# Kernel tuning notes

Measured on AMD Instinct MI355X. Metric: run time of the kernel, lower is better.

The kernel has to match this reference:

```python
import jax, jax.numpy as jnp
import numpy as np

HIDDEN = 2048
KEY_DIM = 2048
NUM_HEADS = 16
EPS = 1e-05


def rms_norm(x, w, eps=EPS):
    ms = jnp.mean(x * x, axis=-1, keepdims=True)
    return x * jax.lax.rsqrt(ms + eps) * w


def setup_inputs() -> dict:
    key = jax.random.key(0)
    ks = jax.random.split(key, 6)
    bound = 1.0 / np.sqrt(HIDDEN)  # kaiming-uniform-ish scale
    x = jax.random.normal(ks[0], (2, 2048, HIDDEN), dtype=jnp.float32)
    rms_w = jnp.ones((HIDDEN,), dtype=jnp.float32)
    Wq = jax.random.uniform(ks[1], (HIDDEN, KEY_DIM), jnp.float32, -bound, bound)
    Wk = jax.random.uniform(ks[2], (HIDDEN, KEY_DIM), jnp.float32, -bound, bound)
    Wv = jax.random.uniform(ks[3], (HIDDEN, KEY_DIM), jnp.float32, -bound, bound)
    Wo = jax.random.uniform(ks[4], (KEY_DIM, HIDDEN), jnp.float32, -bound, bound)
    return {"x": x, "rms_w": rms_w, "Wq": Wq, "Wk": Wk, "Wv": Wv, "Wo": Wo}


def reference(x, rms_w, Wq, Wk, Wv, Wo):
    B, S, _ = x.shape
    residual = x
    xn = rms_norm(x, rms_w)
    # project and split heads: [B,S,H,Dh]
    q = (xn @ Wq).reshape(B, S, NUM_HEADS, KEY_DIM // NUM_HEADS)
    k = (xn @ Wk).reshape(B, S, NUM_HEADS, KEY_DIM // NUM_HEADS)
    v = (xn @ Wv).reshape(B, S, NUM_HEADS, KEY_DIM // NUM_HEADS)
    # NOTE: original scales by 1/sqrt(key_dim), not head_dim — kept faithful
    scale = 1.0 / jnp.sqrt(jnp.float32(KEY_DIM))
    scores = jnp.einsum('bshd,bthd->bhst', q, k) * scale  # [B,H,S,S]
    causal = jnp.tril(jnp.ones((S, S), dtype=bool))
    scores = jnp.where(causal[None, None], scores, -jnp.inf)
    probs = jax.nn.softmax(scores, axis=-1)  # stable max-subtract internally
    out = jnp.einsum('bhst,bthd->bshd', probs, v).reshape(B, S, KEY_DIM)
    return out @ Wo + residual
```

## Files before the change

kernel.cpp:

```cpp
#include <hip/hip_runtime.h>
#include <math.h>

typedef __attribute__((ext_vector_type(8))) short bf16x8;
typedef __attribute__((ext_vector_type(4))) float f32x4;
typedef __attribute__((ext_vector_type(16))) float f32x16;

#define HID 2048
#define SEQ 2048
#define NH  16
#define DH  128
#define QS_LOG2E 0.0318793607f

__device__ __forceinline__ ushort f2bf(float f) {
  union { float f; unsigned u; } v; v.f = f;
  unsigned r = v.u + 0x7fffu + ((v.u >> 16) & 1u);
  return (ushort)(r >> 16);
}

__device__ __forceinline__ void gload16(const ushort* g, ushort* l) {
  __builtin_amdgcn_global_load_lds((const __attribute__((address_space(1))) void*)g,
                                   (__attribute__((address_space(3))) void*)l,
                                   16, 0, 0);
}

#define VMCNT(n) asm volatile("s_waitcnt vmcnt(" #n ")" ::: "memory")
#define ABAR()   asm volatile("s_barrier" ::: "memory")

__global__ __launch_bounds__(256) void k_transpose4(const float* __restrict__ W0,
                                                    const float* __restrict__ W1,
                                                    const float* __restrict__ W2,
                                                    const float* __restrict__ W3,
                                                    ushort* __restrict__ T0,
                                                    ushort* __restrict__ T3) {
  __shared__ float t[32][33];
  int z = blockIdx.z;
  const float* W = (z == 0) ? W0 : (z == 1) ? W1 : (z == 2) ? W2 : W3;
  ushort* Wt = (z == 3) ? T3 : (T0 + (size_t)z * 2048 * 2048);
  int n0 = blockIdx.x * 32, k0 = blockIdx.y * 32;
  int tx = threadIdx.x, ty = threadIdx.y;
  for (int i = ty; i < 32; i += 8)
    t[i][tx] = W[(size_t)(k0 + i) * HID + n0 + tx];
  __syncthreads();
  for (int i = ty; i < 32; i += 8)
    Wt[(size_t)(n0 + i) * HID + k0 + tx] = f2bf(t[tx][i]);
}

__global__ __launch_bounds__(256) void k_rmsnorm(const float* __restrict__ x,
                                                 const float* __restrict__ w,
                                                 ushort* __restrict__ xn) {
  int row = blockIdx.x;
  const float* xr = x + (size_t)row * HID;
  int base = threadIdx.x * 8;
  float4 a = *(const float4*)(xr + base);
  float4 c = *(const float4*)(xr + base + 4);
  float ss = a.x*a.x + a.y*a.y + a.z*a.z + a.w*a.w
           + c.x*c.x + c.y*c.y + c.z*c.z + c.w*c.w;
  #pragma unroll
  for (int off = 32; off > 0; off >>= 1) ss += __shfl_xor(ss, off);
  __shared__ float red[4];
  if ((threadIdx.x & 63) == 0) red[threadIdx.x >> 6] = ss;
  __syncthreads();
  float tot = red[0] + red[1] + red[2] + red[3];
  float sc = rsqrtf(tot * (1.0f / HID) + 1e-5f);
  float4 wa = *(const float4*)(w + base);
  float4 wc = *(const float4*)(w + base + 4);
  ushort h[8];
  h[0] = f2bf(a.x * sc * wa.x); h[1] = f2bf(a.y * sc * wa.y);
  h[2] = f2bf(a.z * sc * wa.z); h[3] = f2bf(a.w * sc * wa.w);
  h[4] = f2bf(c.x * sc * wc.x); h[5] = f2bf(c.y * sc * wc.y);
  h[6] = f2bf(c.z * sc * wc.z); h[7] = f2bf(c.w * sc * wc.w);
  int4 pk;
  pk.x = h[0] | ((int)h[1] << 16);
  pk.y = h[2] | ((int)h[3] << 16);
  pk.z = h[4] | ((int)h[5] << 16);
  pk.w = h[6] | ((int)h[7] << 16);
  *(int4*)&xn[(size_t)row * HID + base] = pk;
}

__global__ __launch_bounds__(512, 2) void k_gemm10(const ushort* __restrict__ A,
                                                   const ushort* __restrict__ Bt,
                                                   ushort* __restrict__ obf,
                                                   ushort* __restrict__ vt) {
  constexpr int K = 2048;
  __shared__ ushort lds[8][8192];
  const int tid = threadIdx.x;
  const int lane = tid & 63, w = tid >> 6;
  const int wm = w >> 2, wn = w & 3;
  const int g = lane >> 4, l15 = lane & 15;
  const int bm = blockIdx.y, bn = blockIdx.x;

  f32x4 acc[8][4];
  #pragma unroll
  for (int i = 0; i < 8; ++i)
    #pragma unroll
    for (int j = 0; j < 4; ++j) acc[i][j] = f32x4{0.f, 0.f, 0.f, 0.f};

  const ushort* pA[2][2];
  const ushort* pB[2][2];
  #pragma unroll
  for (int kh = 0; kh < 2; ++kh)
    #pragma unroll
    for (int L = 0; L < 2; ++L) {
      int row = L * 128 + w * 16 + (lane >> 2);
      int ck = (lane & 3) ^ ((row >> 1) & 3);
      pA[kh][L] = &A[(size_t)(bm * 256 + row) * K + kh * 32 + ck * 8];
      pB[kh][L] = &Bt[(size_t)(bn * 256 + row) * K + kh * 32 + ck * 8];
    }

  auto STAGE = [&](int buf, int kh) {
    ushort* ra = lds[buf * 4 + kh * 2 + 0];
    ushort* rb = lds[buf * 4 + kh * 2 + 1];
    #pragma unroll
    for (int L = 0; L < 2; ++L) {
      gload16(pA[kh][L], ra + (L * 8 + w) * 512);
      pA[kh][L] += 64;
    }
    #pragma unroll
    for (int L = 0; L < 2; ++L) {
      gload16(pB[kh][L], rb + (L * 8 + w) * 512);
      pB[kh][L] += 64;
    }
  };

  auto COMP = [&](int buf, int kh) {
    const ushort* ra = lds[buf * 4 + kh * 2 + 0];
    const ushort* rb = lds[buf * 4 + kh * 2 + 1];
    bf16x8 aF[8], bF[4];
    #pragma unroll
    for (int i = 0; i < 8; ++i) {
      int row = wm * 128 + i * 16 + l15;
      aF[i] = *(const bf16x8*)&ra[row * 32 + ((g ^ ((row >> 1) & 3)) * 8)];
    }
    #pragma unroll
    for (int j = 0; j < 4; ++j) {
      int row = wn * 64 + j * 16 + l15;
      bF[j] = *(const bf16x8*)&rb[row * 32 + ((g ^ ((row >> 1) & 3)) * 8)];
    }
    __builtin_amdgcn_s_setprio(1);
    #pragma unroll
    for (int i = 0; i < 8; ++i)
      #pragma unroll
      for (int j = 0; j < 4; ++j)
        acc[i][j] = __builtin_amdgcn_mfma_f32_16x16x32_bf16(aF[i], bF[j], acc[i][j], 0, 0, 0);
    __builtin_amdgcn_s_setprio(0);
  };

  STAGE(0, 0); STAGE(0, 1); STAGE(1, 0);

  #pragma unroll 1
  for (int t = 0; t < 30; ++t) {
    const int b = t & 1, nb = b ^ 1;
    VMCNT(8); ABAR();
    STAGE(nb, 1);
    COMP(b, 0);
    VMCNT(8); ABAR();
    STAGE(b, 0);
    COMP(b, 1);
  }
  VMCNT(8); ABAR(); STAGE(1, 1); COMP(0, 0);
  VMCNT(8); ABAR();               COMP(0, 1);
  VMCNT(4); ABAR(); COMP(1, 0);
  VMCNT(0); ABAR(); COMP(1, 1);

  int rbase = bm * 256 + wm * 128 + g * 4;
  int cbase = bn * 256 + wn * 64 + l15;
  if (bn < 16) {
    const float sc = (bn < 8) ? QS_LOG2E : 1.0f;
    #pragma unroll
    for (int i = 0; i < 8; ++i) {
      #pragma unroll
      for (int j = 0; j < 4; ++j) {
        int col = cbase + j * 16;
        #pragma unroll
        for (int r = 0; r < 4; ++r) {
          int row = rbase + i * 16 + r;
          obf[(size_t)row * 4096 + col] = f2bf(acc[i][j][r] * sc);
        }
      }
    }
  } else {
    #pragma unroll
    for (int i = 0; i < 8; ++i) {
      int rowb = rbase + i * 16;
      int b = rowb >> 11, s = rowb & 2047;
      #pragma unroll
      for (int j = 0; j < 4; ++j) {
        int nv = cbase + j * 16 - 4096;
        int h = nv >> 7, d = nv & 127;
        uint lo = (uint)f2bf(acc[i][j][0]) | ((uint)f2bf(acc[i][j][1]) << 16);
        uint hi = (uint)f2bf(acc[i][j][2]) | ((uint)f2bf(acc[i][j][3]) << 16);
        uint2 pk = {lo, hi};
        *(uint2*)&vt[(size_t)((b * NH + h) * DH + d) * SEQ + s] = pk;
      }
    }
  }
}

__global__ __launch_bounds__(256) void k_gemm7o(const ushort* __restrict__ A,
                                                const ushort* __restrict__ Bt,
                                                float* __restrict__ ofl,
                                                const float* __restrict__ resid,
                                                int K) {
  __shared__ ushort sA[128 * 64];
  __shared__ ushort sB[128 * 64];
  const int tid = threadIdx.x;
  const int lane = tid & 63, w = tid >> 6;
  const int wr = w >> 1, wc = w & 1;
  const int bm = blockIdx.y, bn = blockIdx.x;
  const int g = lane >> 4, l15 = lane & 15;
  f32x4 acc[4][4];
  #pragma unroll
  for (int i = 0; i < 4; ++i)
    #pragma unroll
    for (int j = 0; j < 4; ++j) acc[i][j] = f32x4{0.f, 0.f, 0.f, 0.f};

  const ushort* ap[4];
  const ushort* bp[4];
  ushort* la[4];
  ushort* lb[4];
  #pragma unroll
  for (int c = 0; c < 4; ++c) {
    int id = (w * 4 + c) * 64 + lane;
    int r = id >> 3, ck = id & 7;
    int ke = (ck ^ (r & 7)) * 8;
    ap[c] = &A[(size_t)(bm * 128 + r) * K + ke];
    bp[c] = &Bt[(size_t)(bn * 128 + r) * K + ke];
    la[c] = ((ushort*)sA) + (w * 4 + c) * 512;
    lb[c] = ((ushort*)sB) + (w * 4 + c) * 512;
  }

  const int nt = K / 64;
  #pragma unroll 1
  for (int t = 0; t < nt; ++t) {
    #pragma unroll
    for (int c = 0; c < 4; ++c) {
      gload16(ap[c], la[c]);
      gload16(bp[c], lb[c]);
      ap[c] += 64;
      bp[c] += 64;
    }
    __syncthreads();
    #pragma unroll
    for (int kk = 0; kk < 2; ++kk) {
      bf16x8 aF[4], bF[4];
      #pragma unroll
      for (int i = 0; i < 4; ++i) {
        int row = wr * 64 + i * 16 + l15;
        int cp = (kk * 4 + g) ^ (lane & 7);
        aF[i] = *(const bf16x8*)&sA[row * 64 + cp * 8];
      }
      #pragma unroll
      for (int j = 0; j < 4; ++j) {
        int row = wc * 64 + j * 16 + l15;
        int cp = (kk * 4 + g) ^ (lane & 7);
        bF[j] = *(const bf16x8*)&sB[row * 64 + cp * 8];
      }
      #pragma unroll
      for (int i = 0; i < 4; ++i)
        #pragma unroll
        for (int j = 0; j < 4; ++j)
          acc[i][j] = __builtin_amdgcn_mfma_f32_16x16x32_bf16(aF[i], bF[j], acc[i][j], 0, 0, 0);
    }
    __syncthreads();
  }

  int rbase = bm * 128 + wr * 64 + g * 4;
  int cbase = bn * 128 + wc * 64 + l15;
  #pragma unroll
  for (int i = 0; i < 4; ++i) {
    #pragma unroll
    for (int j = 0; j < 4; ++j) {
      int col = cbase + j * 16;
      #pragma unroll
      for (int r = 0; r < 4; ++r) {
        int row = rbase + i * 16 + r;
        ofl[(size_t)row * HID + col] = acc[i][j][r] + resid[(size_t)row * HID + col];
      }
    }
  }
}

__global__ __launch_bounds__(256, 2) void k_attn5(const ushort* __restrict__ qk,
                                                  const ushort* __restrict__ vt,
                                                  ushort* __restrict__ aout) {
  __shared__ ushort sK[64 * 128];
  __shared__ ushort sV[128 * 64];
  const int tid = threadIdx.x;
  const int lane = tid & 63, w = tid >> 6;
  const int h2 = lane >> 5;
  const int l31 = lane & 31;
  const int bid = blockIdx.x;
  const int t = bid >> 3;
  const int u = t & 31, v = t >> 5;
  const int bh = (bid & 7) + 8 * (u & 3);
  const int qblk = v ? 15 - (u >> 2) : (u >> 2);
  const int b = bh >> 4, hh = bh & 15;
  const int q0w = qblk * 128 + w * 32;

  bf16x8 qf[8];
  {
    const ushort* qbase = qk + (size_t)(b * SEQ + q0w + l31) * 4096 + hh * DH;
    #pragma unroll
    for (int kk = 0; kk < 8; ++kk) qf[kk] = *(const bf16x8*)&qbase[kk * 16 + h2 * 8];
  }

  const ushort* kp[4];
  const ushort* vp[4];
  ushort* lk[4];
  ushort* lv[4];
  #pragma unroll
  for (int c = 0; c < 4; ++c) {
    int id = (w * 4 + c) * 64 + lane;
    int kr = id >> 4, ck = id & 15;
    kp[c] = qk + (size_t)(b * SEQ + kr) * 4096 + 2048 + hh * DH + ((ck ^ (kr & 7)) * 8);
    int dr = id >> 3, cv = id & 7;
    vp[c] = vt + (size_t)(bh * DH + dr) * SEQ + ((cv ^ (dr & 7)) * 8);
    lk[c] = ((ushort*)sK) + (size_t)(w * 4 + c) * 512;
    lv[c] = ((ushort*)sV) + (size_t)(w * 4 + c) * 512;
  }

  f32x16 accO[4];
  #pragma unroll
  for (int i = 0; i < 4; ++i)
    #pragma unroll
    for (int r = 0; r < 16; ++r) accO[i][r] = 0.f;
  float l_r = 0.f;

  const int ntile = 2 * qblk + 2;
  #pragma unroll 1
  for (int tt = 0; tt < ntile; ++tt) {
    const int t0 = tt * 64;
    #pragma unroll
    for (int c = 0; c < 4; ++c) {
      gload16(kp[c], lk[c]);
      gload16(vp[c], lv[c]);
      kp[c] += 64 * 4096;
      vp[c] += 64;
    }
    __syncthreads();

    if (t0 <= q0w + 31) {
      f32x16 accS[2];
      #pragma unroll
      for (int i = 0; i < 2; ++i)
        #pragma unroll
        for (int r = 0; r < 16; ++r) accS[i][r] = 0.f;
      #pragma unroll
      for (int kt = 0; kt < 2; ++kt) {
        const int row = kt * 32 + l31;
        #pragma unroll
        for (int kk = 0; kk < 8; ++kk) {
          const int cp = (kk * 2 + h2) ^ (lane & 7);
          bf16x8 kf = *(const bf16x8*)&sK[row * 128 + cp * 8];
          accS[kt] = __builtin_amdgcn_mfma_f32_32x32x16_bf16(kf, qf[kk], accS[kt], 0, 0, 0);
        }
      }
      float rs = 0.f;
      if (t0 + 63 <= q0w) {
        #pragma unroll
        for (int kt = 0; kt < 2; ++kt)
          #pragma unroll
          for (int r = 0; r < 16; ++r) {
            float p = __builtin_amdgcn_exp2f(accS[kt][r]);
            rs += p;
            accS[kt][r] = p;
          }
      } else {
        const int qa = q0w + l31;
        #pragma unroll
        for (int kt = 0; kt < 2; ++kt)
          #pragma unroll
          for (int r = 0; r < 16; ++r) {
            int ka = t0 + kt * 32 + (r & 3) + 8 * (r >> 2) + 4 * h2;
            float p = (ka <= qa) ? __builtin_amdgcn_exp2f(accS[kt][r]) : 0.f;
            rs += p;
            accS[kt][r] = p;
          }
      }
      rs += __shfl_xor(rs, 32);
      l_r += rs;

      uint W[2][4][2];
      #pragma unroll
      for (int kt = 0; kt < 2; ++kt)
        #pragma unroll
        for (int bq = 0; bq < 4; ++bq)
          #pragma unroll
          for (int w2 = 0; w2 < 2; ++w2) {
            uint u0 = __float_as_uint(accS[kt][bq * 4 + w2 * 2]);
            uint u1 = __float_as_uint(accS[kt][bq * 4 + w2 * 2 + 1]);
            W[kt][bq][w2] = (u0 >> 16) | (u1 & 0xffff0000u);
          }
      #pragma unroll
      for (int kc = 0; kc < 4; ++kc) {
        const int kt = kc >> 1, pq = kc & 1;
        uint X0 = W[kt][2 * pq][0],     X1 = W[kt][2 * pq][1];
        uint Y0 = W[kt][2 * pq + 1][0], Y1 = W[kt][2 * pq + 1][1];
        uint sx0 = (uint)__shfl_xor((int)X0, 32);
        uint sx1 = (uint)__shfl_xor((int)X1, 32);
        uint sy0 = (uint)__shfl_xor((int)Y0, 32);
        uint sy1 = (uint)__shfl_xor((int)Y1, 32);
        union { uint u[4]; bf16x8 v; } pu;
        pu.u[0] = h2 ? sy0 : X0;
        pu.u[1] = h2 ? sy1 : X1;
        pu.u[2] = h2 ? Y0 : sx0;
        pu.u[3] = h2 ? Y1 : sx1;
        #pragma unroll
        for (int ds = 0; ds < 4; ++ds) {
          const int dr = ds * 32 + l31;
          const int cp = (kc * 2 + h2) ^ (lane & 7);
          bf16x8 vf = *(const bf16x8*)&sV[dr * 64 + cp * 8];
          accO[ds] = __builtin_amdgcn_mfma_f32_32x32x16_bf16(pu.v, vf, accO[ds], 0, 0, 0);
        }
      }
    }
    __syncthreads();
  }

  float linv = 1.f / l_r;
  #pragma unroll
  for (int r = 0; r < 16; ++r) {
    int qrel = (r & 3) + 8 * (r >> 2) + 4 * h2;
    float li = __shfl(linv, qrel);
    #pragma unroll
    for (int ds = 0; ds < 4; ++ds) {
      aout[(size_t)(b * SEQ + q0w + qrel) * HID + hh * DH + ds * 32 + l31] =
          f2bf(accO[ds][r] * li);
    }
  }
}

extern "C" void kernel_launch(void* const* d_in, const int* in_sizes, int n_in,
                              void* d_out, int out_size, void* d_ws, size_t ws_size,
                              hipStream_t stream) {
  const float* x     = (const float*)d_in[0];
  const float* rms_w = (const float*)d_in[1];
  const float* Wq    = (const float*)d_in[2];
  const float* Wk    = (const float*)d_in[3];
  const float* Wv    = (const float*)d_in[4];
  const float* Wo    = (const float*)d_in[5];
  float* out = (float*)d_out;

  char* ws = (char*)d_ws;
  ushort* WqkvT = (ushort*)ws; ws += (size_t)6144 * 2048 * 2;
  ushort* WoT   = (ushort*)ws; ws += (size_t)2048 * 2048 * 2;
  ushort* xn    = (ushort*)ws; ws += (size_t)4096 * 2048 * 2;
  ushort* qkbuf = (ushort*)ws; ws += (size_t)4096 * 4096 * 2;
  ushort* vt    = (ushort*)ws; ws += (size_t)4096 * 2048 * 2;
  ushort* aout  = (ushort*)ws; ws += (size_t)4096 * 2048 * 2;

  k_transpose4<<<dim3(64, 64, 4), dim3(32, 8), 0, stream>>>(Wq, Wk, Wv, Wo, WqkvT, WoT);

  k_rmsnorm<<<4096, 256, 0, stream>>>(x, rms_w, xn);

  k_gemm10<<<dim3(24, 16), 512, 0, stream>>>(xn, WqkvT, qkbuf, vt);

  k_attn5<<<512, 256, 0, stream>>>(qkbuf, vt, aout);

  k_gemm7o<<<dim3(16, 32), 256, 0, stream>>>(aout, WoT, out, x, 2048);
}
```

Baseline: 260.3 us.

## Split QKV GEMM compute into half-tiles interleaved with global-to-LDS staging

Restructures the QKV projection GEMM main loop so each K-step is split into two halves. Each half reads part of the A fragments from LDS, issues half of the next global-to-LDS loads, then runs 16 MFMAs, with extra barriers and explicit lgkmcnt waits between phases. The aim is to spread memory issue across the compute so loads and MFMAs overlap better, and to hold fewer A fragments in registers at once. The cost is many more s_barrier instructions per iteration, which can add stalls across the 8 waves.

```diff
diff --git a/kernel.cpp b/kernel.cpp
--- a/kernel.cpp
+++ b/kernel.cpp
@@ -24,6 +24,8 @@
 }
 
 #define VMCNT(n) asm volatile("s_waitcnt vmcnt(" #n ")" ::: "memory")
+#define LGKM0()  do { asm volatile("s_waitcnt lgkmcnt(0)" ::: "memory"); \
+                      __builtin_amdgcn_sched_barrier(0); } while (0)
 #define ABAR()   asm volatile("s_barrier" ::: "memory")
 
 __global__ __launch_bounds__(256) void k_transpose4(const float* __restrict__ W0,
@@ -77,7 +79,7 @@
   *(int4*)&xn[(size_t)row * HID + base] = pk;
 }
 
-__global__ __launch_bounds__(512, 2) void k_gemm10(const ushort* __restrict__ A,
+__global__ __launch_bounds__(512, 2) void k_gemm11(const ushort* __restrict__ A,
                                                    const ushort* __restrict__ Bt,
                                                    ushort* __restrict__ obf,
                                                    ushort* __restrict__ vt) {
@@ -107,60 +109,100 @@
       pB[kh][L] = &Bt[(size_t)(bn * 256 + row) * K + kh * 32 + ck * 8];
     }
 
-  auto STAGE = [&](int buf, int kh) {
+  bf16x8 aF[4], aH[4], bF[4];
+
+  auto stageA = [&](int buf, int kh) {
     ushort* ra = lds[buf * 4 + kh * 2 + 0];
-    ushort* rb = lds[buf * 4 + kh * 2 + 1];
     #pragma unroll
     for (int L = 0; L < 2; ++L) {
       gload16(pA[kh][L], ra + (L * 8 + w) * 512);
       pA[kh][L] += 64;
     }
+  };
+  auto stageB = [&](int buf, int kh) {
+    ushort* rb = lds[buf * 4 + kh * 2 + 1];
     #pragma unroll
     for (int L = 0; L < 2; ++L) {
       gload16(pB[kh][L], rb + (L * 8 + w) * 512);
       pB[kh][L] += 64;
     }
   };
-
-  auto COMP = [&](int buf, int kh) {
+  auto dsAlo = [&](int buf, int kh) {
     const ushort* ra = lds[buf * 4 + kh * 2 + 0];
-    const ushort* rb = lds[buf * 4 + kh * 2 + 1];
-    bf16x8 aF[8], bF[4];
-    #pragma unroll
-    for (int i = 0; i < 8; ++i) {
+    #pragma unroll
+    for (int i = 0; i < 4; ++i) {
       int row = wm * 128 + i * 16 + l15;
       aF[i] = *(const bf16x8*)&ra[row * 32 + ((g ^ ((row >> 1) & 3)) * 8)];
     }
+  };
+  auto dsAhi = [&](int buf, int kh) {
+    const ushort* ra = lds[buf * 4 + kh * 2 + 0];
+    #pragma unroll
+    for (int i = 0; i < 4; ++i) {
+      int row = wm * 128 + (i + 4) * 16 + l15;
+      aH[i] = *(const bf16x8*)&ra[row * 32 + ((g ^ ((row >> 1) & 3)) * 8)];
+    }
+  };
+  auto dsB4 = [&](int buf, int kh) {
+    const ushort* rb = lds[buf * 4 + kh * 2 + 1];
     #pragma unroll
     for (int j = 0; j < 4; ++j) {
       int row = wn * 64 + j * 16 + l15;
       bF[j] = *(const bf16x8*)&rb[row * 32 + ((g ^ ((row >> 1) & 3)) * 8)];
     }
+  };
+  auto MMlo = [&]() {
     __builtin_amdgcn_s_setprio(1);
     #pragma unroll
-    for (int i = 0; i < 8; ++i)
+    for (int i = 0; i < 4; ++i)
       #pragma unroll
       for (int j = 0; j < 4; ++j)
         acc[i][j] = __builtin_amdgcn_mfma_f32_16x16x32_bf16(aF[i], bF[j], acc[i][j], 0, 0, 0);
     __builtin_amdgcn_s_setprio(0);
   };
-
-  STAGE(0, 0); STAGE(0, 1); STAGE(1, 0);
+  auto MMhi = [&]() {
+    __builtin_amdgcn_s_setprio(1);
+    #pragma unroll
+    for (int i = 0; i < 4; ++i)
+      #pragma unroll
+      for (int j = 0; j < 4; ++j)
+        acc[4 + i][j] = __builtin_amdgcn_mfma_f32_16x16x32_bf16(aH[i], bF[j], acc[4 + i][j], 0, 0, 0);
+    __builtin_amdgcn_s_setprio(0);
+  };
+
+  stageA(0, 0); stageB(0, 0);
+  stageA(0, 1); stageB(0, 1);
+  stageA(1, 0); stageB(1, 0);
+  VMCNT(8); ABAR();
 
   #pragma unroll 1
   for (int t = 0; t < 30; ++t) {
     const int b = t & 1, nb = b ^ 1;
-    VMCNT(8); ABAR();
-    STAGE(nb, 1);
-    COMP(b, 0);
-    VMCNT(8); ABAR();
-    STAGE(b, 0);
-    COMP(b, 1);
-  }
-  VMCNT(8); ABAR(); STAGE(1, 1); COMP(0, 0);
-  VMCNT(8); ABAR();               COMP(0, 1);
-  VMCNT(4); ABAR(); COMP(1, 0);
-  VMCNT(0); ABAR(); COMP(1, 1);
+    dsAlo(b, 0); dsB4(b, 0); stageA(nb, 1);
+    ABAR(); LGKM0(); MMlo(); ABAR();
+    dsAhi(b, 0); stageB(nb, 1);
+    ABAR(); LGKM0(); MMhi(); VMCNT(8); ABAR();
+    dsAlo(b, 1); dsB4(b, 1); stageA(b, 0);
+    ABAR(); LGKM0(); MMlo(); ABAR();
+    dsAhi(b, 1); stageB(b, 0);
+    ABAR(); LGKM0(); MMhi(); VMCNT(8); ABAR();
+  }
+  dsAlo(0, 0); dsB4(0, 0); stageA(1, 1);
+  ABAR(); LGKM0(); MMlo(); ABAR();
+  dsAhi(0, 0); stageB(1, 1);
+  ABAR(); LGKM0(); MMhi(); VMCNT(8); ABAR();
+  dsAlo(0, 1); dsB4(0, 1);
+  ABAR(); LGKM0(); MMlo(); ABAR();
+  dsAhi(0, 1);
+  ABAR(); LGKM0(); MMhi(); VMCNT(4); ABAR();
+  dsAlo(1, 0); dsB4(1, 0);
+  ABAR(); LGKM0(); MMlo(); ABAR();
+  dsAhi(1, 0);
+  ABAR(); LGKM0(); MMhi(); VMCNT(0); ABAR();
+  dsAlo(1, 1); dsB4(1, 1);
+  ABAR(); LGKM0(); MMlo(); ABAR();
+  dsAhi(1, 1);
+  LGKM0(); MMhi();
 
   int rbase = bm * 256 + wm * 128 + g * 4;
   int cbase = bn * 256 + wn * 64 + l15;
@@ -453,7 +495,7 @@
 
   k_rmsnorm<<<4096, 256, 0, stream>>>(x, rms_w, xn);
 
-  k_gemm10<<<dim3(24, 16), 512, 0, stream>>>(xn, WqkvT, qkbuf, vt);
+  k_gemm11<<<dim3(24, 16), 512, 0, stream>>>(xn, WqkvT, qkbuf, vt);
 
   k_attn5<<<512, 256, 0, stream>>>(qkbuf, vt, aout);
 
```

Result: no change. 261.8 us (+0.6%).

## Double-buffer K/V tiles in attention and merge transpose with rmsnorm launch

Applied to the files above, without the earlier changes.

The attention kernel now keeps two LDS buffers for K and V. The next tile's global-to-LDS loads are issued before the current tile is computed, with vmcnt waits and raw barriers replacing __syncthreads, so load latency overlaps with MFMA work. Separately, the weight transpose and RMSNorm kernels are merged into a single launch using an extra z slice, which removes one kernel launch. Doubling LDS to 64KB per block may reduce occupancy, and the hand-counted vmcnt must match the number of outstanding loads.

```diff
diff --git a/kernel.cpp b/kernel.cpp
--- a/kernel.cpp
+++ b/kernel.cpp
@@ -26,55 +26,57 @@
 #define VMCNT(n) asm volatile("s_waitcnt vmcnt(" #n ")" ::: "memory")
 #define ABAR()   asm volatile("s_barrier" ::: "memory")
 
-__global__ __launch_bounds__(256) void k_transpose4(const float* __restrict__ W0,
-                                                    const float* __restrict__ W1,
-                                                    const float* __restrict__ W2,
-                                                    const float* __restrict__ W3,
-                                                    ushort* __restrict__ T0,
-                                                    ushort* __restrict__ T3) {
-  __shared__ float t[32][33];
-  int z = blockIdx.z;
-  const float* W = (z == 0) ? W0 : (z == 1) ? W1 : (z == 2) ? W2 : W3;
-  ushort* Wt = (z == 3) ? T3 : (T0 + (size_t)z * 2048 * 2048);
-  int n0 = blockIdx.x * 32, k0 = blockIdx.y * 32;
-  int tx = threadIdx.x, ty = threadIdx.y;
-  for (int i = ty; i < 32; i += 8)
-    t[i][tx] = W[(size_t)(k0 + i) * HID + n0 + tx];
-  __syncthreads();
-  for (int i = ty; i < 32; i += 8)
-    Wt[(size_t)(n0 + i) * HID + k0 + tx] = f2bf(t[tx][i]);
-}
-
-__global__ __launch_bounds__(256) void k_rmsnorm(const float* __restrict__ x,
-                                                 const float* __restrict__ w,
-                                                 ushort* __restrict__ xn) {
-  int row = blockIdx.x;
-  const float* xr = x + (size_t)row * HID;
-  int base = threadIdx.x * 8;
-  float4 a = *(const float4*)(xr + base);
-  float4 c = *(const float4*)(xr + base + 4);
-  float ss = a.x*a.x + a.y*a.y + a.z*a.z + a.w*a.w
-           + c.x*c.x + c.y*c.y + c.z*c.z + c.w*c.w;
-  #pragma unroll
-  for (int off = 32; off > 0; off >>= 1) ss += __shfl_xor(ss, off);
-  __shared__ float red[4];
-  if ((threadIdx.x & 63) == 0) red[threadIdx.x >> 6] = ss;
-  __syncthreads();
-  float tot = red[0] + red[1] + red[2] + red[3];
-  float sc = rsqrtf(tot * (1.0f / HID) + 1e-5f);
-  float4 wa = *(const float4*)(w + base);
-  float4 wc = *(const float4*)(w + base + 4);
-  ushort h[8];
-  h[0] = f2bf(a.x * sc * wa.x); h[1] = f2bf(a.y * sc * wa.y);
-  h[2] = f2bf(a.z * sc * wa.z); h[3] = f2bf(a.w * sc * wa.w);
-  h[4] = f2bf(c.x * sc * wc.x); h[5] = f2bf(c.y * sc * wc.y);
-  h[6] = f2bf(c.z * sc * wc.z); h[7] = f2bf(c.w * sc * wc.w);
-  int4 pk;
-  pk.x = h[0] | ((int)h[1] << 16);
-  pk.y = h[2] | ((int)h[3] << 16);
-  pk.z = h[4] | ((int)h[5] << 16);
-  pk.w = h[6] | ((int)h[7] << 16);
-  *(int4*)&xn[(size_t)row * HID + base] = pk;
+__global__ __launch_bounds__(256) void k_prep(const float* __restrict__ W0,
+                                              const float* __restrict__ W1,
+                                              const float* __restrict__ W2,
+                                              const float* __restrict__ W3,
+                                              ushort* __restrict__ T0,
+                                              ushort* __restrict__ T3,
+                                              const float* __restrict__ x,
+                                              const float* __restrict__ rw,
+                                              ushort* __restrict__ xn) {
+  const int z = blockIdx.z;
+  if (z < 4) {
+    __shared__ float t[32][33];
+    const float* W = (z == 0) ? W0 : (z == 1) ? W1 : (z == 2) ? W2 : W3;
+    ushort* Wt = (z == 3) ? T3 : (T0 + (size_t)z * 2048 * 2048);
+    int n0 = blockIdx.x * 32, k0 = blockIdx.y * 32;
+    int tx = threadIdx.x, ty = threadIdx.y;
+    for (int i = ty; i < 32; i += 8)
+      t[i][tx] = W[(size_t)(k0 + i) * HID + n0 + tx];
+    __syncthreads();
+    for (int i = ty; i < 32; i += 8)
+      Wt[(size_t)(n0 + i) * HID + k0 + tx] = f2bf(t[tx][i]);
+  } else {
+    const int tid = threadIdx.y * 32 + threadIdx.x;
+    const int row = blockIdx.y * 64 + blockIdx.x;
+    const float* xr = x + (size_t)row * HID;
+    int base = tid * 8;
+    float4 a = *(const float4*)(xr + base);
+    float4 c = *(const float4*)(xr + base + 4);
+    float ss = a.x*a.x + a.y*a.y + a.z*a.z + a.w*a.w
+             + c.x*c.x + c.y*c.y + c.z*c.z + c.w*c.w;
+    #pragma unroll
+    for (int off = 32; off > 0; off >>= 1) ss += __shfl_xor(ss, off);
+    __shared__ float red[4];
+    if ((tid & 63) == 0) red[tid >> 6] = ss;
+    __syncthreads();
+    float tot = red[0] + red[1] + red[2] + red[3];
+    float sc = rsqrtf(tot * (1.0f / HID) + 1e-5f);
+    float4 wa = *(const float4*)(rw + base);
+    float4 wc = *(const float4*)(rw + base + 4);
+    ushort h[8];
+    h[0] = f2bf(a.x * sc * wa.x); h[1] = f2bf(a.y * sc * wa.y);
+    h[2] = f2bf(a.z * sc * wa.z); h[3] = f2bf(a.w * sc * wa.w);
+    h[4] = f2bf(c.x * sc * wc.x); h[5] = f2bf(c.y * sc * wc.y);
+    h[6] = f2bf(c.z * sc * wc.z); h[7] = f2bf(c.w * sc * wc.w);
+    int4 pk;
+    pk.x = h[0] | ((int)h[1] << 16);
+    pk.y = h[2] | ((int)h[3] << 16);
+    pk.z = h[4] | ((int)h[5] << 16);
+    pk.w = h[6] | ((int)h[7] << 16);
+    *(int4*)&xn[(size_t)row * HID + base] = pk;
+  }
 }
 
 __global__ __launch_bounds__(512, 2) void k_gemm10(const ushort* __restrict__ A,
@@ -280,11 +282,11 @@
   }
 }
 
-__global__ __launch_bounds__(256, 2) void k_attn5(const ushort* __restrict__ qk,
+__global__ __launch_bounds__(256, 2) void k_attn6(const ushort* __restrict__ qk,
                                                   const ushort* __restrict__ vt,
                                                   ushort* __restrict__ aout) {
-  __shared__ ushort sK[64 * 128];
-  __shared__ ushort sV[128 * 64];
+  __shared__ ushort sK[2][64 * 128];
+  __shared__ ushort sV[2][128 * 64];
   const int tid = threadIdx.x;
   const int lane = tid & 63, w = tid >> 6;
   const int h2 = lane >> 5;
@@ -306,8 +308,7 @@
 
   const ushort* kp[4];
   const ushort* vp[4];
-  ushort* lk[4];
-  ushort* lv[4];
+  int lofs[4];
   #pragma unroll
   for (int c = 0; c < 4; ++c) {
     int id = (w * 4 + c) * 64 + lane;
@@ -315,9 +316,18 @@
     kp[c] = qk + (size_t)(b * SEQ + kr) * 4096 + 2048 + hh * DH + ((ck ^ (kr & 7)) * 8);
     int dr = id >> 3, cv = id & 7;
     vp[c] = vt + (size_t)(bh * DH + dr) * SEQ + ((cv ^ (dr & 7)) * 8);
-    lk[c] = ((ushort*)sK) + (size_t)(w * 4 + c) * 512;
-    lv[c] = ((ushort*)sV) + (size_t)(w * 4 + c) * 512;
-  }
+    lofs[c] = (w * 4 + c) * 512;
+  }
+
+  auto STAGE = [&](int buf) {
+    #pragma unroll
+    for (int c = 0; c < 4; ++c) {
+      gload16(kp[c], &sK[buf][0] + lofs[c]);
+      gload16(vp[c], &sV[buf][0] + lofs[c]);
+      kp[c] += 64 * 4096;
+      vp[c] += 64;
+    }
+  };
 
   f32x16 accO[4];
   #pragma unroll
@@ -326,96 +336,96 @@
     for (int r = 0; r < 16; ++r) accO[i][r] = 0.f;
   float l_r = 0.f;
 
-  const int ntile = 2 * qblk + 2;
-  #pragma unroll 1
-  for (int tt = 0; tt < ntile; ++tt) {
+  auto COMPUTE = [&](int tt, int buf) {
     const int t0 = tt * 64;
-    #pragma unroll
-    for (int c = 0; c < 4; ++c) {
-      gload16(kp[c], lk[c]);
-      gload16(vp[c], lv[c]);
-      kp[c] += 64 * 4096;
-      vp[c] += 64;
-    }
-    __syncthreads();
-
-    if (t0 <= q0w + 31) {
-      f32x16 accS[2];
-      #pragma unroll
-      for (int i = 0; i < 2; ++i)
-        #pragma unroll
-        for (int r = 0; r < 16; ++r) accS[i][r] = 0.f;
-      #pragma unroll
-      for (int kt = 0; kt < 2; ++kt) {
-        const int row = kt * 32 + l31;
-        #pragma unroll
-        for (int kk = 0; kk < 8; ++kk) {
-          const int cp = (kk * 2 + h2) ^ (lane & 7);
-          bf16x8 kf = *(const bf16x8*)&sK[row * 128 + cp * 8];
-          accS[kt] = __builtin_amdgcn_mfma_f32_32x32x16_bf16(kf, qf[kk], accS[kt], 0, 0, 0);
-        }
-      }
-      float rs = 0.f;
-      if (t0 + 63 <= q0w) {
-        #pragma unroll
-        for (int kt = 0; kt < 2; ++kt)
-          #pragma unroll
-          for (int r = 0; r < 16; ++r) {
-            float p = __builtin_amdgcn_exp2f(accS[kt][r]);
-            rs += p;
-            accS[kt][r] = p;
-          }
-      } else {
-        const int qa = q0w + l31;
-        #pragma unroll
-        for (int kt = 0; kt < 2; ++kt)
-          #pragma unroll
-          for (int r = 0; r < 16; ++r) {
-            int ka = t0 + kt * 32 + (r & 3) + 8 * (r >> 2) + 4 * h2;
-            float p = (ka <= qa) ? __builtin_amdgcn_exp2f(accS[kt][r]) : 0.f;
-            rs += p;
-            accS[kt][r] = p;
-          }
-      }
-      rs += __shfl_xor(rs, 32);
-      l_r += rs;
-
-      uint W[2][4][2];
+    f32x16 accS[2];
+    #pragma unroll
+    for (int i = 0; i < 2; ++i)
+      #pragma unroll
+      for (int r = 0; r < 16; ++r) accS[i][r] = 0.f;
+    #pragma unroll
+    for (int kt = 0; kt < 2; ++kt) {
+      const int row = kt * 32 + l31;
+      #pragma unroll
+      for (int kk = 0; kk < 8; ++kk) {
+        const int cp = (kk * 2 + h2) ^ (lane & 7);
+        bf16x8 kf = *(const bf16x8*)&sK[buf][row * 128 + cp * 8];
+        accS[kt] = __builtin_amdgcn_mfma_f32_32x32x16_bf16(kf, qf[kk], accS[kt], 0, 0, 0);
+      }
+    }
+    float rs = 0.f;
+    if (t0 + 63 <= q0w) {
       #pragma unroll
       for (int kt = 0; kt < 2; ++kt)
         #pragma unroll
-        for (int bq = 0; bq < 4; ++bq)
-          #pragma unroll
-          for (int w2 = 0; w2 < 2; ++w2) {
-            uint u0 = __float_as_uint(accS[kt][bq * 4 + w2 * 2]);
-            uint u1 = __float_as_uint(accS[kt][bq * 4 + w2 * 2 + 1]);
-            W[kt][bq][w2] = (u0 >> 16) | (u1 & 0xffff0000u);
-          }
-      #pragma unroll
-      for (int kc = 0; kc < 4; ++kc) {
-        const int kt = kc >> 1, pq = kc & 1;
-        uint X0 = W[kt][2 * pq][0],     X1 = W[kt][2 * pq][1];
-        uint Y0 = W[kt][2 * pq + 1][0], Y1 = W[kt][2 * pq + 1][1];
-        uint sx0 = (uint)__shfl_xor((int)X0, 32);
-        uint sx1 = (uint)__shfl_xor((int)X1, 32);
-        uint sy0 = (uint)__shfl_xor((int)Y0, 32);
-        uint sy1 = (uint)__shfl_xor((int)Y1, 32);
-        union { uint u[4]; bf16x8 v; } pu;
-        pu.u[0] = h2 ? sy0 : X0;
-        pu.u[1] = h2 ? sy1 : X1;
-        pu.u[2] = h2 ? Y0 : sx0;
-        pu.u[3] = h2 ? Y1 : sx1;
+        for (int r = 0; r < 16; ++r) {
+          float p = __builtin_amdgcn_exp2f(accS[kt][r]);
+          rs += p;
+          accS[kt][r] = p;
+        }
+    } else {
+      const int qa = q0w + l31;
+      #pragma unroll
+      for (int kt = 0; kt < 2; ++kt)
         #pragma unroll
-        for (int ds = 0; ds < 4; ++ds) {
-          const int dr = ds * 32 + l31;
-          const int cp = (kc * 2 + h2) ^ (lane & 7);
-          bf16x8 vf = *(const bf16x8*)&sV[dr * 64 + cp * 8];
-          accO[ds] = __builtin_amdgcn_mfma_f32_32x32x16_bf16(pu.v, vf, accO[ds], 0, 0, 0);
+        for (int r = 0; r < 16; ++r) {
+          int ka = t0 + kt * 32 + (r & 3) + 8 * (r >> 2) + 4 * h2;
+          float p = (ka <= qa) ? __builtin_amdgcn_exp2f(accS[kt][r]) : 0.f;
+          rs += p;
+          accS[kt][r] = p;
         }
-      }
-    }
-    __syncthreads();
-  }
+    }
+    rs += __shfl_xor(rs, 32);
+    l_r += rs;
+
+    uint W[2][4][2];
+    #pragma unroll
+    for (int kt = 0; kt < 2; ++kt)
+      #pragma unroll
+      for (int bq = 0; bq < 4; ++bq)
+        #pragma unroll
+        for (int w2 = 0; w2 < 2; ++w2) {
+          uint u0 = __float_as_uint(accS[kt][bq * 4 + w2 * 2]);
+          uint u1 = __float_as_uint(accS[kt][bq * 4 + w2 * 2 + 1]);
+          W[kt][bq][w2] = (u0 >> 16) | (u1 & 0xffff0000u);
+        }
+    #pragma unroll
+    for (int kc = 0; kc < 4; ++kc) {
+      const int kt = kc >> 1, pq = kc & 1;
+      uint X0 = W[kt][2 * pq][0],     X1 = W[kt][2 * pq][1];
+      uint Y0 = W[kt][2 * pq + 1][0], Y1 = W[kt][2 * pq + 1][1];
+      uint sx0 = (uint)__shfl_xor((int)X0, 32);
+      uint sx1 = (uint)__shfl_xor((int)X1, 32);
+      uint sy0 = (uint)__shfl_xor((int)Y0, 32);
+      uint sy1 = (uint)__shfl_xor((int)Y1, 32);
+      union { uint u[4]; bf16x8 v; } pu;
+      pu.u[0] = h2 ? sy0 : X0;
+      pu.u[1] = h2 ? sy1 : X1;
+      pu.u[2] = h2 ? Y0 : sx0;
+      pu.u[3] = h2 ? Y1 : sx1;
+      #pragma unroll
+      for (int ds = 0; ds < 4; ++ds) {
+        const int dr = ds * 32 + l31;
+        const int cp = (kc * 2 + h2) ^ (lane & 7);
+        bf16x8 vf = *(const bf16x8*)&sV[buf][dr * 64 + cp * 8];
+        accO[ds] = __builtin_amdgcn_mfma_f32_32x32x16_bf16(pu.v, vf, accO[ds], 0, 0, 0);
+      }
+    }
+  };
+
+  const int ntile = 2 * qblk + 2;
+  STAGE(0);
+  #pragma unroll 1
+  for (int tt = 0; tt < ntile - 1; ++tt) {
+    STAGE((tt + 1) & 1);
+    VMCNT(8);
+    ABAR();
+    if (tt * 64 <= q0w + 31) COMPUTE(tt, tt & 1);
+    ABAR();
+  }
+  VMCNT(0);
+  ABAR();
+  if ((ntile - 1) * 64 <= q0w + 31) COMPUTE(ntile - 1, (ntile - 1) & 1);
 
   float linv = 1.f / l_r;
   #pragma unroll
@@ -449,13 +459,12 @@
   ushort* vt    = (ushort*)ws; ws += (size_t)4096 * 2048 * 2;
   ushort* aout  = (ushort*)ws; ws += (size_t)4096 * 2048 * 2;
 
-  k_transpose4<<<dim3(64, 64, 4), dim3(32, 8), 0, stream>>>(Wq, Wk, Wv, Wo, WqkvT, WoT);
-
-  k_rmsnorm<<<4096, 256, 0, stream>>>(x, rms_w, xn);
+  k_prep<<<dim3(64, 64, 5), dim3(32, 8), 0, stream>>>(Wq, Wk, Wv, Wo, WqkvT, WoT,
+                                                      x, rms_w, xn);
 
   k_gemm10<<<dim3(24, 16), 512, 0, stream>>>(xn, WqkvT, qkbuf, vt);
 
-  k_attn5<<<512, 256, 0, stream>>>(qkbuf, vt, aout);
+  k_attn6<<<512, 256, 0, stream>>>(qkbuf, vt, aout);
 
   k_gemm7o<<<dim3(16, 32), 256, 0, stream>>>(aout, WoT, out, x, 2048);
 }
```

Result: no change. 255.6 us (-1.8%).
